# Optimization experiments

Measured on AMD Instinct MI355X. Metric: run time of the kernel, lower is better.

Reference implementation:

```python
import jax, jax.numpy as jnp
import numpy as np

DIM = 768
HEADS = 12
DIM_HEAD = DIM // HEADS
SEQ = 1024
BATCH = 16
DEPTH = 6
MAX_DEPTH = 12
ALPHA = 0.5


def _decomposed_kernel(n, depth, alpha, max_depth, inverse):
    # symmetric (inverse) matrix square root of the OU-process kernel matrix
    if depth == 0:
        return np.eye(n, dtype=np.float32)
    gamma = -0.5 * np.log(1.0 - alpha ** (2.0 * depth / max_depth))
    ar = np.arange(n, dtype=np.float64)
    K = np.exp(-gamma * np.abs(ar[:, None] - ar[None, :]))
    w, V = np.linalg.eigh(K)
    thr = w.max() * n * np.finfo(w.dtype).eps
    s = np.clip(w, thr, None)
    s = 1.0 / np.sqrt(s) if inverse else np.sqrt(s)
    return ((V * s[None, :]) @ V.T).astype(np.float32)


def _make_buffers():
    prev_inv = _decomposed_kernel(SEQ, DEPTH - 1, ALPHA, MAX_DEPTH, inverse=True)
    cur = _decomposed_kernel(SEQ, DEPTH, ALPHA, MAX_DEPTH, inverse=False)
    A = (cur @ prev_inv).astype(np.float32)
    mn = A.min()
    if mn <= 0:
        A = np.clip(A, abs(mn) + np.finfo(np.float32).eps, None)
    row_sum = A.sum(1)                      # (N,)
    B = np.log(A / row_sum)                 # broadcast over last axis (matches torch)
    d = row_sum.reshape(1, 1, SEQ, 1).astype(np.float32)
    return jnp.asarray(d), jnp.asarray(B[None, None]).astype(jnp.float32)


def setup_inputs() -> dict:
    key = jax.random.key(0)
    kx, kw = jax.random.split(key)
    x = jax.random.normal(kx, (BATCH, SEQ, DIM), dtype=jnp.float32)
    # module zeros the q block; use normal(std=dim^-0.5) everywhere for a non-degenerate test
    w_qkv = jax.random.normal(kw, (3 * DIM, DIM), dtype=jnp.float32) * (DIM ** -0.5)
    b_qkv = jnp.zeros((3 * DIM,), dtype=jnp.float32)
    d, b_bias = _make_buffers()
    return {"x": x, "w_qkv": w_qkv, "b_qkv": b_qkv, "d": d, "b_bias": b_bias}


def reference(x, w_qkv, b_qkv, d, b_bias):
    B, N, D = x.shape
    qkv = x @ w_qkv.T + b_qkv                                   # (B,N,3D)
    qkv = qkv.reshape(B, N, 3, HEADS, DIM_HEAD).transpose(2, 0, 3, 1, 4)
    q, k, v = qkv[0], qkv[1], qkv[2]                            # (B,H,N,dh)
    scale = DIM_HEAD ** -0.5
    scores = jnp.einsum("bhnd,bhmd->bhnm", q, k) * scale + b_bias
    attn = jax.nn.softmax(scores, axis=-1)
    out = d * jnp.einsum("bhnm,bhmd->bhnd", attn, v)            # post-softmax row scale
    return out.transpose(0, 2, 1, 3).reshape(B, N, D)
```

## Files before the change

### kernel.cpp

```cpp
#include <hip/hip_runtime.h>
#include <cstdint>
#include <cstddef>

typedef __attribute__((ext_vector_type(8))) short short8;
typedef __attribute__((ext_vector_type(4))) short short4_;
typedef __attribute__((ext_vector_type(4))) float f32x4;
typedef __attribute__((ext_vector_type(2))) unsigned int uint2_;

__device__ inline unsigned short bf16rne(float f) {
    uint32_t u = __builtin_bit_cast(uint32_t, f);
    u += 0x7fffu + ((u >> 16) & 1u);
    return (unsigned short)(u >> 16);
}

#define GLDS(g, l)                                                              \
    __builtin_amdgcn_global_load_lds(                                           \
        (const __attribute__((address_space(1))) void*)(g),                     \
        (__attribute__((address_space(3))) void*)(l), 16, 0, 0)

__global__ void cvt_kernel(const float* __restrict__ src,
                           unsigned short* __restrict__ dst, int n8) {
    int i = blockIdx.x * blockDim.x + threadIdx.x;
    if (i >= n8) return;
    const float4* s = (const float4*)src + (size_t)i * 2;
    float4 a = s[0], b = s[1];
    uint32_t w0 = bf16rne(a.x) | ((uint32_t)bf16rne(a.y) << 16);
    uint32_t w1 = bf16rne(a.z) | ((uint32_t)bf16rne(a.w) << 16);
    uint32_t w2 = bf16rne(b.x) | ((uint32_t)bf16rne(b.y) << 16);
    uint32_t w3 = bf16rne(b.z) | ((uint32_t)bf16rne(b.w) << 16);
    uint4 o; o.x = w0; o.y = w1; o.z = w2; o.w = w3;
    ((uint4*)dst)[i] = o;
}

__global__ __launch_bounds__(256) void qkv_gemm(
    const unsigned short* __restrict__ X, const unsigned short* __restrict__ W,
    const float* __restrict__ bqkv,
    unsigned short* __restrict__ qo, unsigned short* __restrict__ ko,
    unsigned short* __restrict__ vo)
{
    __shared__ unsigned short smem[16896];
    unsigned short* As = smem;
    unsigned short* Bs = smem + 8192;

    const int tid  = threadIdx.x;
    const int m0   = blockIdx.y * 128;
    const int n0   = blockIdx.x * 128;
    const int wid  = tid >> 6;
    const int lane = tid & 63;
    const int m16  = lane & 15;
    const int quad = lane >> 4;
    const int wm   = wid >> 1, wn = wid & 1;

    f32x4 acc[4][4];
    #pragma unroll
    for (int i = 0; i < 4; i++)
        #pragma unroll
        for (int j = 0; j < 4; j++) acc[i][j] = (f32x4){0.f, 0.f, 0.f, 0.f};

    for (int kt = 0; kt < 12; ++kt) {
        const int k0 = kt * 64;
        #pragma unroll
        for (int rd = 0; rd < 4; ++rd) {
            int id = rd * 256 + tid;
            int row = id >> 3, c = id & 7;
            GLDS(X + (size_t)(m0 + row) * 768 + k0 + c * 8, &As[id * 8]);
        }
        #pragma unroll
        for (int rd = 0; rd < 4; ++rd) {
            int id = rd * 256 + tid;
            int row = id >> 3, c = id & 7;
            GLDS(W + (size_t)(n0 + row) * 768 + k0 + c * 8, &Bs[id * 8]);
        }
        __syncthreads();
        #pragma unroll
        for (int ks = 0; ks < 2; ++ks) {
            short8 a[4], b[4];
            #pragma unroll
            for (int mb = 0; mb < 4; mb++)
                a[mb] = *(const short8*)&As[(wm * 64 + mb * 16 + m16) * 64 + ks * 32 + quad * 8];
            #pragma unroll
            for (int nb = 0; nb < 4; nb++)
                b[nb] = *(const short8*)&Bs[(wn * 64 + nb * 16 + m16) * 64 + ks * 32 + quad * 8];
            #pragma unroll
            for (int mb = 0; mb < 4; mb++)
                #pragma unroll
                for (int nb = 0; nb < 4; nb++)
                    acc[mb][nb] = __builtin_amdgcn_mfma_f32_16x16x32_bf16(
                        a[mb], b[nb], acc[mb][nb], 0, 0, 0);
        }
        __syncthreads();
    }

    float bias_n[4];
    #pragma unroll
    for (int nb = 0; nb < 4; nb++) bias_n[nb] = bqkv[n0 + wn * 64 + nb * 16 + m16];

    const int which = n0 / 768;
    const int hbase = (n0 % 768) / 64;
    const int bI  = m0 >> 10;
    const int ns0 = m0 & 1023;

    if (which == 2) {
        #pragma unroll
        for (int mb = 0; mb < 4; ++mb)
            #pragma unroll
            for (int nb = 0; nb < 4; ++nb) {
                int n  = wn * 64 + nb * 16 + m16;
                int hh = hbase + (n >> 6);
                int d  = n & 63;
                int pos = ns0 + wm * 64 + mb * 16 + quad * 4;
                short4_ v4;
                #pragma unroll
                for (int r = 0; r < 4; ++r)
                    v4[r] = (short)bf16rne(acc[mb][nb][r] + bias_n[nb]);
                *(short4_*)(vo + ((size_t)(bI * 12 + hh) * 64 + d) * 1024 + pos) = v4;
            }
        return;
    }

    #pragma unroll
    for (int mb = 0; mb < 4; mb++)
        #pragma unroll
        for (int nb = 0; nb < 4; nb++)
            #pragma unroll
            for (int r = 0; r < 4; r++) {
                float v = acc[mb][nb][r] + bias_n[nb];
                smem[(wm * 64 + mb * 16 + quad * 4 + r) * 132 + wn * 64 + nb * 16 + m16] =
                    bf16rne(v);
            }
    __syncthreads();

    unsigned short* outp = (which == 0) ? qo : ko;
    #pragma unroll
    for (int rd = 0; rd < 8; ++rd) {
        int id = rd * 256 + tid;
        int row = id >> 4, c = id & 15;
        short4_ lo = *(const short4_*)&smem[row * 132 + c * 8];
        short4_ hi = *(const short4_*)&smem[row * 132 + c * 8 + 4];
        short8 v8 = __builtin_shufflevector(lo, hi, 0, 1, 2, 3, 4, 5, 6, 7);
        int h  = hbase + (c >> 3);
        int dc = (c & 7) * 8;
        unsigned short* dst =
            outp + ((size_t)(bI * 12 + h) * 1024 + ns0 + row) * 64 + dc;
        *(short8*)dst = v8;
    }
}

__global__ __launch_bounds__(512, 4) void attn_kernel(
    const unsigned short* __restrict__ Q, const unsigned short* __restrict__ K,
    const unsigned short* __restrict__ Vt, const float* __restrict__ bias,
    const float* __restrict__ dvec, float* __restrict__ out, int nbh8)
{
    __shared__ unsigned short Ks[2][4096];
    __shared__ unsigned short Vs[2][4096];

    const int tid  = threadIdx.x;
    const int wid  = tid >> 6;
    const int lane = tid & 63;
    const int m16  = lane & 15;
    const int quad = lane >> 4;

    const int f    = blockIdx.x;
    const int xcd  = f & 7;
    const int r_   = f >> 3;
    const int qt   = r_ & 7;
    const int bhl  = r_ >> 3;
    const int bh   = xcd * nbh8 + bhl;
    const int b = bh / 12, h = bh % 12;
    const int q0 = qt * 128;
    const int qrow = q0 + wid * 16 + m16;

    const unsigned short* Qb = Q  + (size_t)bh * 65536;
    const unsigned short* Kb = K  + (size_t)bh * 65536;
    const unsigned short* Vb = Vt + (size_t)bh * 65536;
    const float* brow = bias + (size_t)qrow * 1024 + quad * 4;

    int k_src, v_src;
    {
        int pos = tid >> 3, dbs = tid & 7;
        int db = dbs ^ (pos & 7);
        k_src = pos * 64 + db * 8;
        int pb = tid >> 6, d = tid & 63;
        v_src = d * 1024 + pb * 8;
    }

    short8 qf0 = *(const short8*)(Qb + (size_t)qrow * 64 + quad * 8);
    short8 qf1 = *(const short8*)(Qb + (size_t)qrow * 64 + 32 + quad * 8);

    f32x4 acc[4];
    #pragma unroll
    for (int nb = 0; nb < 4; nb++) acc[nb] = (f32x4){0.f, 0.f, 0.f, 0.f};
    float m_i = -3.0e38f, l_i = 0.f;

    GLDS(Kb + k_src, &Ks[0][tid * 8]);
    GLDS(Vb + v_src, &Vs[0][tid * 8]);
    float4 bv[4];
    #pragma unroll
    for (int cb = 0; cb < 4; ++cb) bv[cb] = *(const float4*)(brow + cb * 16);
    __syncthreads();

    for (int kv = 0; kv < 16; ++kv) {
        const int cur = kv & 1;
        const int k0n = (kv + 1) * 64;

        f32x4 sc[4];
        #pragma unroll
        for (int cb = 0; cb < 4; ++cb) {
            sc[cb][0] = bv[cb].x * 8.0f;
            sc[cb][1] = bv[cb].y * 8.0f;
            sc[cb][2] = bv[cb].z * 8.0f;
            sc[cb][3] = bv[cb].w * 8.0f;
        }

        if (kv < 15) {
            GLDS(Kb + (size_t)k0n * 64 + k_src, &Ks[cur ^ 1][tid * 8]);
            GLDS(Vb + (size_t)k0n + v_src, &Vs[cur ^ 1][tid * 8]);
            #pragma unroll
            for (int cb = 0; cb < 4; ++cb)
                bv[cb] = *(const float4*)(brow + k0n + cb * 16);
        }

        #pragma unroll
        for (int ks = 0; ks < 2; ++ks) {
            #pragma unroll
            for (int cb = 0; cb < 4; ++cb) {
                int pos = cb * 16 + m16;
                int slot = pos * 8 + ((ks * 4 + quad) ^ (m16 & 7));
                short8 a = *(const short8*)&Ks[cur][slot * 8];
                sc[cb] = __builtin_amdgcn_mfma_f32_16x16x32_bf16(
                    a, (ks == 0) ? qf0 : qf1, sc[cb], 0, 0, 0);
            }
        }

        float mx = -3.0e38f;
        #pragma unroll
        for (int cb = 0; cb < 4; ++cb) {
            sc[cb][0] *= 0.125f;
            sc[cb][1] *= 0.125f;
            sc[cb][2] *= 0.125f;
            sc[cb][3] *= 0.125f;
            mx = fmaxf(mx, fmaxf(fmaxf(sc[cb][0], sc[cb][1]), fmaxf(sc[cb][2], sc[cb][3])));
        }
        mx = fmaxf(mx, __shfl_xor(mx, 16, 64));
        mx = fmaxf(mx, __shfl_xor(mx, 32, 64));

        if (!__all(mx <= m_i)) {
            float mnew = fmaxf(m_i, mx);
            float al = __expf(m_i - mnew);
            m_i = mnew;
            l_i *= al;
            #pragma unroll
            for (int nb = 0; nb < 4; nb++) {
                acc[nb][0] *= al; acc[nb][1] *= al;
                acc[nb][2] *= al; acc[nb][3] *= al;
            }
        }

        float rs = 0.f;
        short4_ pf[4];
        #pragma unroll
        for (int cb = 0; cb < 4; ++cb) {
            float p0 = __expf(sc[cb][0] - m_i);
            float p1 = __expf(sc[cb][1] - m_i);
            float p2 = __expf(sc[cb][2] - m_i);
            float p3 = __expf(sc[cb][3] - m_i);
            rs += (p0 + p1) + (p2 + p3);
            uint2_ pd;
            pd[0] = __builtin_amdgcn_perm(__builtin_bit_cast(uint32_t, p1),
                                          __builtin_bit_cast(uint32_t, p0), 0x07060302u);
            pd[1] = __builtin_amdgcn_perm(__builtin_bit_cast(uint32_t, p3),
                                          __builtin_bit_cast(uint32_t, p2), 0x07060302u);
            pf[cb] = __builtin_bit_cast(short4_, pd);
        }
        rs += __shfl_xor(rs, 16, 64);
        rs += __shfl_xor(rs, 32, 64);
        l_i += rs;

        #pragma unroll
        for (int ks = 0; ks < 4; ++ks) {
            #pragma unroll
            for (int nb = 0; nb < 4; ++nb) {
                int slot = (ks * 2 + (quad >> 1)) * 64 + nb * 16 + m16;
                short4_ av = *(const short4_*)&Vs[cur][slot * 8 + (quad & 1) * 4];
                acc[nb] = __builtin_amdgcn_mfma_f32_16x16x16bf16_1k(av, pf[ks], acc[nb], 0, 0, 0);
            }
        }

        __syncthreads();
    }

    float scl = dvec[qrow] / l_i;
    #pragma unroll
    for (int nb = 0; nb < 4; ++nb) {
        float4 o;
        o.x = acc[nb][0] * scl; o.y = acc[nb][1] * scl;
        o.z = acc[nb][2] * scl; o.w = acc[nb][3] * scl;
        *(float4*)(out + ((size_t)b * 1024 + qrow) * 768 + h * 64 + nb * 16 + quad * 4) = o;
    }
}

extern "C" void kernel_launch(void* const* d_in, const int* in_sizes, int n_in,
                              void* d_out, int out_size, void* d_ws, size_t ws_size,
                              hipStream_t stream) {
    const float* x     = (const float*)d_in[0];
    const float* w     = (const float*)d_in[1];
    const float* bqkv  = (const float*)d_in[2];
    const float* dvec  = (const float*)d_in[3];
    const float* bbias = (const float*)d_in[4];
    float* out = (float*)d_out;

    char* ws = (char*)d_ws;
    unsigned short* wb = (unsigned short*)ws;
    unsigned short* xb = (unsigned short*)((char*)d_out + 25165824);

    cvt_kernel<<<6144, 256, 0, stream>>>(x, xb, 1572864);
    cvt_kernel<<<864, 256, 0, stream>>>(w, wb, 221184);

    const size_t NEED_FULL = 3538944ull + 3ull * 25165824ull;
    if (ws_size >= NEED_FULL) {
        unsigned short* qb = (unsigned short*)(ws + 3538944);
        unsigned short* kb = qb + 12582912;
        unsigned short* vb = kb + 12582912;
        qkv_gemm<<<dim3(18, 128), 256, 0, stream>>>(xb, wb, bqkv, qb, kb, vb);
        attn_kernel<<<1536, 512, 0, stream>>>(qb, kb, vb, bbias, dvec, out, 24);
    } else {
        unsigned short* qb = (unsigned short*)(ws + 3538944);
        unsigned short* kb = qb + 3145728;
        unsigned short* vb = kb + 3145728;
        for (int c = 0; c < 4; ++c) {
            const unsigned short* xc = xb + (size_t)c * 3145728;
            qkv_gemm<<<dim3(18, 32), 256, 0, stream>>>(xc, wb, bqkv, qb, kb, vb);
            attn_kernel<<<384, 512, 0, stream>>>(
                qb, kb, vb, bbias, dvec, out + (size_t)c * 3145728, 6);
        }
    }
}
```

Baseline: 333.5 us.

## Double-buffer QKV GEMM, swizzle LDS, remap blocks, fold scale, use exp2

```diff
diff --git a/kernel.cpp b/kernel.cpp
--- a/kernel.cpp
+++ b/kernel.cpp
@@ -43,8 +43,11 @@
     unsigned short* Bs = smem + 8192;
 
     const int tid  = threadIdx.x;
-    const int m0   = blockIdx.y * 128;
-    const int n0   = blockIdx.x * 128;
+    const int f    = blockIdx.x + gridDim.x * blockIdx.y;
+    const int per  = (gridDim.x * gridDim.y) >> 3;
+    const int wk   = (f & 7) * per + (f >> 3);
+    const int m0   = (wk / 18) * 128;
+    const int n0   = (wk % 18) * 128;
     const int wid  = tid >> 6;
     const int lane = tid & 63;
     const int m16  = lane & 15;
@@ -57,37 +60,46 @@
         #pragma unroll
         for (int j = 0; j < 4; j++) acc[i][j] = (f32x4){0.f, 0.f, 0.f, 0.f};
 
-    for (int kt = 0; kt < 12; ++kt) {
-        const int k0 = kt * 64;
-        #pragma unroll
-        for (int rd = 0; rd < 4; ++rd) {
+    auto stage = [&](int buf, int k0) {
+        #pragma unroll
+        for (int rd = 0; rd < 2; ++rd) {
             int id = rd * 256 + tid;
-            int row = id >> 3, c = id & 7;
-            GLDS(X + (size_t)(m0 + row) * 768 + k0 + c * 8, &As[id * 8]);
-        }
-        #pragma unroll
-        for (int rd = 0; rd < 4; ++rd) {
+            int row = id >> 2;
+            int cs = (id & 3) ^ (row & 3);
+            GLDS(X + (size_t)(m0 + row) * 768 + k0 + cs * 8, &As[buf * 4096 + id * 8]);
+        }
+        #pragma unroll
+        for (int rd = 0; rd < 2; ++rd) {
             int id = rd * 256 + tid;
-            int row = id >> 3, c = id & 7;
-            GLDS(W + (size_t)(n0 + row) * 768 + k0 + c * 8, &Bs[id * 8]);
-        }
-        __syncthreads();
-        #pragma unroll
-        for (int ks = 0; ks < 2; ++ks) {
-            short8 a[4], b[4];
-            #pragma unroll
-            for (int mb = 0; mb < 4; mb++)
-                a[mb] = *(const short8*)&As[(wm * 64 + mb * 16 + m16) * 64 + ks * 32 + quad * 8];
+            int row = id >> 2;
+            int cs = (id & 3) ^ (row & 3);
+            GLDS(W + (size_t)(n0 + row) * 768 + k0 + cs * 8, &Bs[buf * 4096 + id * 8]);
+        }
+    };
+
+    stage(0, 0);
+    __syncthreads();
+
+    const int csw = (quad ^ (m16 & 3)) * 8;
+    for (int kt = 0; kt < 24; ++kt) {
+        const int cur = kt & 1;
+        if (kt < 23) stage(cur ^ 1, (kt + 1) * 32);
+
+        short8 a[4], b[4];
+        #pragma unroll
+        for (int mb = 0; mb < 4; mb++)
+            a[mb] = *(const short8*)&As[cur * 4096 + (wm * 64 + mb * 16 + m16) * 32 + csw];
+        #pragma unroll
+        for (int nb = 0; nb < 4; nb++)
+            b[nb] = *(const short8*)&Bs[cur * 4096 + (wn * 64 + nb * 16 + m16) * 32 + csw];
+        __builtin_amdgcn_s_setprio(1);
+        #pragma unroll
+        for (int mb = 0; mb < 4; mb++)
             #pragma unroll
             for (int nb = 0; nb < 4; nb++)
-                b[nb] = *(const short8*)&Bs[(wn * 64 + nb * 16 + m16) * 64 + ks * 32 + quad * 8];
-            #pragma unroll
-            for (int mb = 0; mb < 4; mb++)
-                #pragma unroll
-                for (int nb = 0; nb < 4; nb++)
-                    acc[mb][nb] = __builtin_amdgcn_mfma_f32_16x16x32_bf16(
-                        a[mb], b[nb], acc[mb][nb], 0, 0, 0);
-        }
+                acc[mb][nb] = __builtin_amdgcn_mfma_f32_16x16x32_bf16(
+                    a[mb], b[nb], acc[mb][nb], 0, 0, 0);
+        __builtin_amdgcn_s_setprio(0);
         __syncthreads();
     }
 
@@ -118,13 +130,14 @@
         return;
     }
 
+    const float qscale = (which == 0) ? 0.125f : 1.0f;
     #pragma unroll
     for (int mb = 0; mb < 4; mb++)
         #pragma unroll
         for (int nb = 0; nb < 4; nb++)
             #pragma unroll
             for (int r = 0; r < 4; r++) {
-                float v = acc[mb][nb][r] + bias_n[nb];
+                float v = (acc[mb][nb][r] + bias_n[nb]) * qscale;
                 smem[(wm * 64 + mb * 16 + quad * 4 + r) * 132 + wn * 64 + nb * 16 + m16] =
                     bf16rne(v);
             }
@@ -191,6 +204,7 @@
     #pragma unroll
     for (int nb = 0; nb < 4; nb++) acc[nb] = (f32x4){0.f, 0.f, 0.f, 0.f};
     float m_i = -3.0e38f, l_i = 0.f;
+    const float L2E = 1.4426950408889634f;
 
     GLDS(Kb + k_src, &Ks[0][tid * 8]);
     GLDS(Vb + v_src, &Vs[0][tid * 8]);
@@ -206,10 +220,10 @@
         f32x4 sc[4];
         #pragma unroll
         for (int cb = 0; cb < 4; ++cb) {
-            sc[cb][0] = bv[cb].x * 8.0f;
-            sc[cb][1] = bv[cb].y * 8.0f;
-            sc[cb][2] = bv[cb].z * 8.0f;
-            sc[cb][3] = bv[cb].w * 8.0f;
+            sc[cb][0] = bv[cb].x;
+            sc[cb][1] = bv[cb].y;
+            sc[cb][2] = bv[cb].z;
+            sc[cb][3] = bv[cb].w;
         }
 
         if (kv < 15) {
@@ -220,6 +234,7 @@
                 bv[cb] = *(const float4*)(brow + k0n + cb * 16);
         }
 
+        __builtin_amdgcn_s_setprio(1);
         #pragma unroll
         for (int ks = 0; ks < 2; ++ks) {
             #pragma unroll
@@ -231,22 +246,18 @@
                     a, (ks == 0) ? qf0 : qf1, sc[cb], 0, 0, 0);
             }
         }
+        __builtin_amdgcn_s_setprio(0);
 
         float mx = -3.0e38f;
         #pragma unroll
-        for (int cb = 0; cb < 4; ++cb) {
-            sc[cb][0] *= 0.125f;
-            sc[cb][1] *= 0.125f;
-            sc[cb][2] *= 0.125f;
-            sc[cb][3] *= 0.125f;
+        for (int cb = 0; cb < 4; ++cb)
             mx = fmaxf(mx, fmaxf(fmaxf(sc[cb][0], sc[cb][1]), fmaxf(sc[cb][2], sc[cb][3])));
-        }
         mx = fmaxf(mx, __shfl_xor(mx, 16, 64));
         mx = fmaxf(mx, __shfl_xor(mx, 32, 64));
 
         if (!__all(mx <= m_i)) {
             float mnew = fmaxf(m_i, mx);
-            float al = __expf(m_i - mnew);
+            float al = __builtin_amdgcn_exp2f((m_i - mnew) * L2E);
             m_i = mnew;
             l_i *= al;
             #pragma unroll
@@ -255,15 +266,16 @@
                 acc[nb][2] *= al; acc[nb][3] *= al;
             }
         }
+        const float nmL = -m_i * L2E;
 
         float rs = 0.f;
         short4_ pf[4];
         #pragma unroll
         for (int cb = 0; cb < 4; ++cb) {
-            float p0 = __expf(sc[cb][0] - m_i);
-            float p1 = __expf(sc[cb][1] - m_i);
-            float p2 = __expf(sc[cb][2] - m_i);
-            float p3 = __expf(sc[cb][3] - m_i);
+            float p0 = __builtin_amdgcn_exp2f(__builtin_fmaf(sc[cb][0], L2E, nmL));
+            float p1 = __builtin_amdgcn_exp2f(__builtin_fmaf(sc[cb][1], L2E, nmL));
+            float p2 = __builtin_amdgcn_exp2f(__builtin_fmaf(sc[cb][2], L2E, nmL));
+            float p3 = __builtin_amdgcn_exp2f(__builtin_fmaf(sc[cb][3], L2E, nmL));
             rs += (p0 + p1) + (p2 + p3);
             uint2_ pd;
             pd[0] = __builtin_amdgcn_perm(__builtin_bit_cast(uint32_t, p1),
@@ -276,6 +288,7 @@
         rs += __shfl_xor(rs, 32, 64);
         l_i += rs;
 
+        __builtin_amdgcn_s_setprio(1);
         #pragma unroll
         for (int ks = 0; ks < 4; ++ks) {
             #pragma unroll
@@ -285,6 +298,7 @@
                 acc[nb] = __builtin_amdgcn_mfma_f32_16x16x16bf16_1k(av, pf[ks], acc[nb], 0, 0, 0);
             }
         }
+        __builtin_amdgcn_s_setprio(0);
 
         __syncthreads();
     }
```

After: 317.3 us. -4.9%, faster.
